# Kernel tuning notes

Measured on AMD Instinct MI355X. Metric: run time of the kernel, lower is better.

## Reference

```python
import jax, jax.numpy as jnp
import numpy as np

H = 8  # hidden_size

def setup_inputs() -> dict:
    key = jax.random.key(0)
    ks = jax.random.split(key, 7)
    B, T, I = 131072, 48, 5
    s = 1.0 / np.sqrt(H)  # torch LSTM/Linear init scale (uniform bound); use scaled normal
    return {
        "x": jax.random.normal(ks[0], (B, T, I), dtype=jnp.float32),
        "W_ih": jax.random.normal(ks[1], (4 * H, I), dtype=jnp.float32) * s,
        "W_hh": jax.random.normal(ks[2], (4 * H, H), dtype=jnp.float32) * s,
        "b_ih": jax.random.normal(ks[3], (4 * H,), dtype=jnp.float32) * s,
        "b_hh": jax.random.normal(ks[4], (4 * H,), dtype=jnp.float32) * s,
        "fc_W": jax.random.normal(ks[5], (1, H * T), dtype=jnp.float32) * (1.0 / np.sqrt(H * T)),
        "fc_b": jax.random.normal(ks[6], (1,), dtype=jnp.float32) * (1.0 / np.sqrt(H * T)),
    }

def _lstm_forward(x, W_ih, W_hh, b_ih, b_hh):
    # x: [B, T, I]. PyTorch gate order: i, f, g, o.
    B, T, _ = x.shape
    # Precompute input projections for all timesteps: [B, T, 4H] -> [T, B, 4H]
    xp = jnp.einsum('bti,gi->btg', x, W_ih) + b_ih + b_hh
    xp = xp.transpose(1, 0, 2)

    def step(carry, xt):
        h, c = carry
        gates = xt + h @ W_hh.T  # [B, 4H]
        i, f, g, o = jnp.split(gates, 4, axis=-1)
        c = jax.nn.sigmoid(f) * c + jax.nn.sigmoid(i) * jnp.tanh(g)
        h = jax.nn.sigmoid(o) * jnp.tanh(c)
        return (h, c), h

    h0 = jnp.zeros((B, H), dtype=x.dtype)
    c0 = jnp.zeros((B, H), dtype=x.dtype)
    _, hs = jax.lax.scan(step, (h0, c0), xp)  # hs: [T, B, H]
    return hs.transpose(1, 0, 2)  # [B, T, H]

def reference(x, W_ih, W_hh, b_ih, b_hh, fc_W, fc_b):
    B, T, _ = x.shape
    lstm_out = _lstm_forward(x, W_ih, W_hh, b_ih, b_hh)  # [B, T, H]
    preds = lstm_out.reshape(B, T * H) @ fc_W.T + fc_b   # [B, 1]
    return preds.reshape(-1)  # [B]
```

## Files before the change

### kernel.cpp

```cpp
#include <hip/hip_runtime.h>

#define TT 48
#define II 5
#define HID 8

typedef float float2v __attribute__((ext_vector_type(2)));

template<int CTRL>
__device__ __forceinline__ float dppf(float v) {
    return __int_as_float(__builtin_amdgcn_update_dpp(0, __float_as_int(v), CTRL, 0xF, 0xF, true));
}
__device__ __forceinline__ float swz4(float v) {
    return __int_as_float(__builtin_amdgcn_ds_swizzle(__float_as_int(v), 0x101F));
}
__device__ __forceinline__ float fexp2(float x) {
    float r;
    asm("v_exp_f32 %0, %1" : "=v"(r) : "v"(x));
    return r;
}
__device__ __forceinline__ float frcp(float x) { return __builtin_amdgcn_rcpf(x); }

__device__ __forceinline__ float2v pkfma(float2v a, float2v b, float2v c) {
    return __builtin_elementwise_fma(a, b, c);
}
__device__ __forceinline__ float2v splat(float v) { return (float2v){v, v}; }

__global__ __launch_bounds__(256, 4) void lstm_fused(
    const float* __restrict__ x,
    const float* __restrict__ W_ih,
    const float* __restrict__ W_hh,
    const float* __restrict__ b_ih,
    const float* __restrict__ b_hh,
    const float* __restrict__ fc_W,
    const float* __restrict__ fc_b,
    float* __restrict__ out, int B)
{
    __shared__ __align__(16) float s_fc[TT * HID];
    const int tid = threadIdx.x;
    for (int i = tid; i < TT * HID; i += 256) s_fc[i] = fc_W[i];
    __syncthreads();

    const int gt = blockIdx.x * 256 + tid;
    const int b = gt >> 3;
    const int q = gt & 7;
    if (b >= B) return;

    const float L2E  = 1.44269504088896340736f;
    const float L2E2 = 2.0f * L2E;

    const int r_i = q, r_f = 8 + q, r_g = 16 + q, r_o = 24 + q;

    float2v wihA[II], wihB[II], whhA[HID], whhB[HID], biasA, biasB;
    #pragma unroll
    for (int i = 0; i < II; ++i) {
        wihA[i] = (float2v){L2E  * W_ih[r_i * II + i], L2E * W_ih[r_f * II + i]};
        wihB[i] = (float2v){L2E2 * W_ih[r_g * II + i], L2E * W_ih[r_o * II + i]};
    }
    #pragma unroll
    for (int m = 0; m < HID; ++m) {
        const int e = q ^ m;
        whhA[m] = (float2v){L2E  * W_hh[r_i * HID + e], L2E * W_hh[r_f * HID + e]};
        whhB[m] = (float2v){L2E2 * W_hh[r_g * HID + e], L2E * W_hh[r_o * HID + e]};
    }
    biasA = (float2v){L2E  * (b_ih[r_i] + b_hh[r_i]), L2E * (b_ih[r_f] + b_hh[r_f])};
    biasB = (float2v){L2E2 * (b_ih[r_g] + b_hh[r_g]), L2E * (b_ih[r_o] + b_hh[r_o])};

    const float* xb = x + (size_t)b * (TT * II);
    float h = 0.f, c = 0.f, acc = 0.f;

    float2v xv[II];
    #pragma unroll
    for (int i = 0; i < II; ++i) xv[i] = splat(xb[i]);

    #pragma unroll 4
    for (int t = 0; t < TT; ++t) {
        float xn[II];
        const int tn = (t < TT - 1) ? t + 1 : t;
        #pragma unroll
        for (int i = 0; i < II; ++i) xn[i] = xb[tn * II + i];

        float2v gA = pkfma(wihA[0], xv[0], biasA);
        float2v gB = pkfma(wihB[0], xv[0], biasB);
        #pragma unroll
        for (int i = 1; i < II; ++i) {
            gA = pkfma(wihA[i], xv[i], gA);
            gB = pkfma(wihB[i], xv[i], gB);
        }

        float ha0 = h;
        float ha1 = dppf<0xB1>(h);
        float ha2 = dppf<0x4E>(h);
        float ha3 = dppf<0x4E>(ha1);
        float ha4 = swz4(ha0), ha5 = swz4(ha1), ha6 = swz4(ha2), ha7 = swz4(ha3);

        gA = pkfma(whhA[0], splat(ha0), gA);  gB = pkfma(whhB[0], splat(ha0), gB);
        gA = pkfma(whhA[1], splat(ha1), gA);  gB = pkfma(whhB[1], splat(ha1), gB);
        gA = pkfma(whhA[2], splat(ha2), gA);  gB = pkfma(whhB[2], splat(ha2), gB);
        gA = pkfma(whhA[3], splat(ha3), gA);  gB = pkfma(whhB[3], splat(ha3), gB);
        gA = pkfma(whhA[4], splat(ha4), gA);  gB = pkfma(whhB[4], splat(ha4), gB);
        gA = pkfma(whhA[5], splat(ha5), gA);  gB = pkfma(whhB[5], splat(ha5), gB);
        gA = pkfma(whhA[6], splat(ha6), gA);  gB = pkfma(whhB[6], splat(ha6), gB);
        gA = pkfma(whhA[7], splat(ha7), gA);  gB = pkfma(whhB[7], splat(ha7), gB);

        const float si = frcp(1.0f + fexp2(-gA.x));
        const float sf = frcp(1.0f + fexp2(-gA.y));
        const float tg = fmaf(-2.0f, frcp(1.0f + fexp2(gB.x)), 1.0f);
        const float so = frcp(1.0f + fexp2(-gB.y));

        c = fmaf(sf, c, si * tg);
        const float tc = fmaf(-2.0f, frcp(1.0f + fexp2(c * L2E2)), 1.0f);
        h = so * tc;

        acc = fmaf(h, s_fc[t * HID + q], acc);

        #pragma unroll
        for (int i = 0; i < II; ++i) xv[i] = splat(xn[i]);
    }

    acc += dppf<0xB1>(acc);
    acc += dppf<0x4E>(acc);
    acc += swz4(acc);
    if (q == 0) out[b] = acc + fc_b[0];
}

extern "C" void kernel_launch(void* const* d_in, const int* in_sizes, int n_in,
                              void* d_out, int out_size, void* d_ws, size_t ws_size,
                              hipStream_t stream) {
    const float* x    = (const float*)d_in[0];
    const float* W_ih = (const float*)d_in[1];
    const float* W_hh = (const float*)d_in[2];
    const float* b_ih = (const float*)d_in[3];
    const float* b_hh = (const float*)d_in[4];
    const float* fc_W = (const float*)d_in[5];
    const float* fc_b = (const float*)d_in[6];
    float* out = (float*)d_out;

    const int B = in_sizes[0] / (TT * II);
    const long long threads = (long long)B * 8;
    const int grid = (int)((threads + 255) / 256);
    lstm_fused<<<grid, 256, 0, stream>>>(x, W_ih, W_hh, b_ih, b_hh, fc_W, fc_b, out, B);
}
```

Baseline: 104.4 us.

## Load x as float4 blocks, replace ds_swizzle with DPP row ops, fold gate negation

Input x is now fetched as five float4 loads per 4-timestep block and prefetched one block ahead, instead of five scalar loads per timestep. The cross-lane h broadcast swaps ds_swizzle (an LDS-path op) for DPP quad-permute and row-half-mirror patterns, which stay in VALU. The sigmoid negation is folded into the pre-scaled weights and biases, and empty asm constraints pin the weights in registers. The prefetch adds register pressure and relies on the DPP patterns delivering the correct partner lanes within each 8-lane group.

```diff
diff --git a/kernel.cpp b/kernel.cpp
--- a/kernel.cpp
+++ b/kernel.cpp
@@ -10,20 +10,16 @@
 __device__ __forceinline__ float dppf(float v) {
     return __int_as_float(__builtin_amdgcn_update_dpp(0, __float_as_int(v), CTRL, 0xF, 0xF, true));
 }
-__device__ __forceinline__ float swz4(float v) {
-    return __int_as_float(__builtin_amdgcn_ds_swizzle(__float_as_int(v), 0x101F));
-}
+
 __device__ __forceinline__ float fexp2(float x) {
-    float r;
-    asm("v_exp_f32 %0, %1" : "=v"(r) : "v"(x));
-    return r;
+    float r; asm("v_exp_f32 %0, %1" : "=v"(r) : "v"(x)); return r;
 }
 __device__ __forceinline__ float frcp(float x) { return __builtin_amdgcn_rcpf(x); }
-
 __device__ __forceinline__ float2v pkfma(float2v a, float2v b, float2v c) {
     return __builtin_elementwise_fma(a, b, c);
 }
 __device__ __forceinline__ float2v splat(float v) { return (float2v){v, v}; }
+__device__ __forceinline__ void pin2(float2v& v) { asm("" : "+v"(v)); }
 
 __global__ __launch_bounds__(256, 4) void lstm_fused(
     const float* __restrict__ x,
@@ -47,79 +43,100 @@
 
     const float L2E  = 1.44269504088896340736f;
     const float L2E2 = 2.0f * L2E;
+    const float sI = -L2E, sF = -L2E, sG = L2E2, sO = -L2E;
 
     const int r_i = q, r_f = 8 + q, r_g = 16 + q, r_o = 24 + q;
 
     float2v wihA[II], wihB[II], whhA[HID], whhB[HID], biasA, biasB;
     #pragma unroll
     for (int i = 0; i < II; ++i) {
-        wihA[i] = (float2v){L2E  * W_ih[r_i * II + i], L2E * W_ih[r_f * II + i]};
-        wihB[i] = (float2v){L2E2 * W_ih[r_g * II + i], L2E * W_ih[r_o * II + i]};
+        wihA[i] = (float2v){sI * W_ih[r_i * II + i], sF * W_ih[r_f * II + i]};
+        wihB[i] = (float2v){sG * W_ih[r_g * II + i], sO * W_ih[r_o * II + i]};
     }
     #pragma unroll
     for (int m = 0; m < HID; ++m) {
         const int e = q ^ m;
-        whhA[m] = (float2v){L2E  * W_hh[r_i * HID + e], L2E * W_hh[r_f * HID + e]};
-        whhB[m] = (float2v){L2E2 * W_hh[r_g * HID + e], L2E * W_hh[r_o * HID + e]};
+        whhA[m] = (float2v){sI * W_hh[r_i * HID + e], sF * W_hh[r_f * HID + e]};
+        whhB[m] = (float2v){sG * W_hh[r_g * HID + e], sO * W_hh[r_o * HID + e]};
     }
-    biasA = (float2v){L2E  * (b_ih[r_i] + b_hh[r_i]), L2E * (b_ih[r_f] + b_hh[r_f])};
-    biasB = (float2v){L2E2 * (b_ih[r_g] + b_hh[r_g]), L2E * (b_ih[r_o] + b_hh[r_o])};
+    biasA = (float2v){sI * (b_ih[r_i] + b_hh[r_i]), sF * (b_ih[r_f] + b_hh[r_f])};
+    biasB = (float2v){sG * (b_ih[r_g] + b_hh[r_g]), sO * (b_ih[r_o] + b_hh[r_o])};
+
+    #pragma unroll
+    for (int i = 0; i < II; ++i) { pin2(wihA[i]); pin2(wihB[i]); }
+    #pragma unroll
+    for (int m = 0; m < HID; ++m) { pin2(whhA[m]); pin2(whhB[m]); }
+    pin2(biasA); pin2(biasB);
 
     const float* xb = x + (size_t)b * (TT * II);
+    const float4* xb4 = reinterpret_cast<const float4*>(xb);
+
     float h = 0.f, c = 0.f, acc = 0.f;
 
-    float2v xv[II];
+    float xc[20];
     #pragma unroll
-    for (int i = 0; i < II; ++i) xv[i] = splat(xb[i]);
+    for (int k = 0; k < 5; ++k) {
+        float4 v = xb4[k];
+        xc[4*k] = v.x; xc[4*k+1] = v.y; xc[4*k+2] = v.z; xc[4*k+3] = v.w;
+    }
 
-    #pragma unroll 4
-    for (int t = 0; t < TT; ++t) {
-        float xn[II];
-        const int tn = (t < TT - 1) ? t + 1 : t;
+    #pragma unroll 1
+    for (int bi = 0; bi < 12; ++bi) {
+        const int nb = (bi < 11) ? bi + 1 : 11;
+        float4 p[5];
         #pragma unroll
-        for (int i = 0; i < II; ++i) xn[i] = xb[tn * II + i];
+        for (int k = 0; k < 5; ++k) p[k] = xb4[nb * 5 + k];
 
-        float2v gA = pkfma(wihA[0], xv[0], biasA);
-        float2v gB = pkfma(wihB[0], xv[0], biasB);
         #pragma unroll
-        for (int i = 1; i < II; ++i) {
-            gA = pkfma(wihA[i], xv[i], gA);
-            gB = pkfma(wihB[i], xv[i], gB);
+        for (int s = 0; s < 4; ++s) {
+            const int t = bi * 4 + s;
+
+            float2v gA = pkfma(wihA[0], splat(xc[s*5 + 0]), biasA);
+            float2v gB = pkfma(wihB[0], splat(xc[s*5 + 0]), biasB);
+            #pragma unroll
+            for (int i = 1; i < II; ++i) {
+                gA = pkfma(wihA[i], splat(xc[s*5 + i]), gA);
+                gB = pkfma(wihB[i], splat(xc[s*5 + i]), gB);
+            }
+
+            const float ha1 = dppf<0xB1>(h);
+            const float ha2 = dppf<0x4E>(h);
+            const float ha3 = dppf<0x1B>(h);
+            const float ha7 = dppf<0x141>(h);
+            const float ha6 = dppf<0x141>(ha1);
+            const float ha5 = dppf<0x141>(ha2);
+            const float ha4 = dppf<0x141>(ha3);
+
+            gA = pkfma(whhA[0], splat(h),   gA);  gB = pkfma(whhB[0], splat(h),   gB);
+            gA = pkfma(whhA[1], splat(ha1), gA);  gB = pkfma(whhB[1], splat(ha1), gB);
+            gA = pkfma(whhA[2], splat(ha2), gA);  gB = pkfma(whhB[2], splat(ha2), gB);
+            gA = pkfma(whhA[3], splat(ha3), gA);  gB = pkfma(whhB[3], splat(ha3), gB);
+            gA = pkfma(whhA[4], splat(ha4), gA);  gB = pkfma(whhB[4], splat(ha4), gB);
+            gA = pkfma(whhA[5], splat(ha5), gA);  gB = pkfma(whhB[5], splat(ha5), gB);
+            gA = pkfma(whhA[6], splat(ha6), gA);  gB = pkfma(whhB[6], splat(ha6), gB);
+            gA = pkfma(whhA[7], splat(ha7), gA);  gB = pkfma(whhB[7], splat(ha7), gB);
+
+            const float si = frcp(1.0f + fexp2(gA.x));
+            const float sf = frcp(1.0f + fexp2(gA.y));
+            const float tg = fmaf(-2.0f, frcp(1.0f + fexp2(gB.x)), 1.0f);
+            const float so = frcp(1.0f + fexp2(gB.y));
+
+            c = fmaf(sf, c, si * tg);
+            const float tc = fmaf(-2.0f, frcp(1.0f + fexp2(c * L2E2)), 1.0f);
+            h = so * tc;
+
+            acc = fmaf(h, s_fc[t * HID + q], acc);
         }
 
-        float ha0 = h;
-        float ha1 = dppf<0xB1>(h);
-        float ha2 = dppf<0x4E>(h);
-        float ha3 = dppf<0x4E>(ha1);
-        float ha4 = swz4(ha0), ha5 = swz4(ha1), ha6 = swz4(ha2), ha7 = swz4(ha3);
-
-        gA = pkfma(whhA[0], splat(ha0), gA);  gB = pkfma(whhB[0], splat(ha0), gB);
-        gA = pkfma(whhA[1], splat(ha1), gA);  gB = pkfma(whhB[1], splat(ha1), gB);
-        gA = pkfma(whhA[2], splat(ha2), gA);  gB = pkfma(whhB[2], splat(ha2), gB);
-        gA = pkfma(whhA[3], splat(ha3), gA);  gB = pkfma(whhB[3], splat(ha3), gB);
-        gA = pkfma(whhA[4], splat(ha4), gA);  gB = pkfma(whhB[4], splat(ha4), gB);
-        gA = pkfma(whhA[5], splat(ha5), gA);  gB = pkfma(whhB[5], splat(ha5), gB);
-        gA = pkfma(whhA[6], splat(ha6), gA);  gB = pkfma(whhB[6], splat(ha6), gB);
-        gA = pkfma(whhA[7], splat(ha7), gA);  gB = pkfma(whhB[7], splat(ha7), gB);
-
-        const float si = frcp(1.0f + fexp2(-gA.x));
-        const float sf = frcp(1.0f + fexp2(-gA.y));
-        const float tg = fmaf(-2.0f, frcp(1.0f + fexp2(gB.x)), 1.0f);
-        const float so = frcp(1.0f + fexp2(-gB.y));
-
-        c = fmaf(sf, c, si * tg);
-        const float tc = fmaf(-2.0f, frcp(1.0f + fexp2(c * L2E2)), 1.0f);
-        h = so * tc;
-
-        acc = fmaf(h, s_fc[t * HID + q], acc);
-
         #pragma unroll
-        for (int i = 0; i < II; ++i) xv[i] = splat(xn[i]);
+        for (int k = 0; k < 5; ++k) {
+            xc[4*k] = p[k].x; xc[4*k+1] = p[k].y; xc[4*k+2] = p[k].z; xc[4*k+3] = p[k].w;
+        }
     }
 
     acc += dppf<0xB1>(acc);
     acc += dppf<0x4E>(acc);
-    acc += swz4(acc);
+    acc += dppf<0x141>(acc);
     if (q == 0) out[b] = acc + fc_b[0];
 }
 
```

After: 105.6 us. Within noise of the previous version (+1.2%).
